# Kernel tuning notes

Measured on AMD Instinct MI355X. Metric: run time of the kernel, lower is better.

Reference implementation:

```python
import jax, jax.numpy as jnp
import numpy as np

B_, C, N, M, DX = 4, 8, 1024, 1024, 1
POINTS_PER_UNIT = 64


def setup_inputs() -> dict:
    key = jax.random.key(0)
    k1, k2, k3 = jax.random.split(key, 3)
    xz = jax.random.uniform(k1, (M, DX), dtype=jnp.float32)          # grid locations
    z = jax.random.normal(k2, (B_, C, M, M), dtype=jnp.float32)      # grid encoding
    x = jax.random.normal(k3, (B_, N, DX), dtype=jnp.float32)        # target locations
    log_scale = jnp.log(jnp.float32(2.0 / POINTS_PER_UNIT))          # learned scalar
    return {"xz": xz, "z": z, "x": x, "log_scale": log_scale}


def reference(xz, z, x, log_scale):
    # pairwise squared distances: (b, n, m)
    dists2 = jnp.sum((x[:, :, None, :] - xz[None, None, :, :]) ** 2, axis=-1)
    # RBF weights
    weights = jnp.exp(-0.5 * dists2 / jnp.exp(2.0 * log_scale))      # (b, n, m)
    # weighted interpolation of grid encoding: (b, c, n, m)
    z1 = jnp.einsum("bnm,bcmk->bcnk", weights, z)
    # outer product z1 @ z1^T: (b, c, n, n)
    z2 = jnp.einsum("bcnk,bcok->bcno", z1, z1)
    return (xz, z2)
```

## Files before the change

kernel.cpp:

```cpp
#include <hip/hip_runtime.h>
#include <hip/hip_bf16.h>


typedef __attribute__((ext_vector_type(8))) unsigned short u16x8;
typedef __attribute__((ext_vector_type(8))) __bf16 bf16x8;
typedef __attribute__((ext_vector_type(4))) float f32x4;

typedef __attribute__((address_space(1))) void gvoid;
typedef __attribute__((address_space(3))) void svoid;
#define GLDS(g, s) __builtin_amdgcn_global_load_lds((gvoid*)(g), (svoid*)(s), 16, 0, 0)
#define BAR() asm volatile("s_barrier" ::: "memory")

__device__ __forceinline__ unsigned short f2bf(float f) {
  unsigned int u = __builtin_bit_cast(unsigned int, f);
  u += 0x7fffu + ((u >> 16) & 1u);
  return (unsigned short)(u >> 16);
}

__device__ __forceinline__ bf16x8 as_bf16x8(u16x8 v) {
  return __builtin_bit_cast(bf16x8, v);
}

__global__ void weights_kernel(const float* __restrict__ xz, const float* __restrict__ x,
                               const float* __restrict__ ls, unsigned short* __restrict__ W) {
  int bn = blockIdx.x;
  float xv = x[bn];
  float coef = -0.5f * __expf(-2.0f * ls[0]);
  unsigned short* Wrow = W + (size_t)bn * 1024;
  #pragma unroll
  for (int i = 0; i < 4; ++i) {
    int m = threadIdx.x + i * 256;
    float d = xv - xz[m];
    Wrow[m] = f2bf(__expf(coef * d * d));
  }
}

__global__ void transpose_kernel(const float* __restrict__ Z, unsigned short* __restrict__ Zt) {
  __shared__ float tile[64][65];
  int bc = blockIdx.z;
  const float* Zp = Z + ((size_t)bc << 20);
  unsigned short* Ztp = Zt + ((size_t)bc << 20);
  int m0 = blockIdx.x * 64, k0 = blockIdx.y * 64;
  int tx = threadIdx.x & 63, tg = threadIdx.x >> 6;
  #pragma unroll
  for (int i = 0; i < 16; ++i) {
    int ml = tg + i * 4;
    tile[ml][tx] = Zp[(size_t)(m0 + ml) * 1024 + k0 + tx];
  }
  __syncthreads();
  int tx2 = (threadIdx.x & 31) * 2, kg = threadIdx.x >> 5;
  #pragma unroll
  for (int i = 0; i < 8; ++i) {
    int kl = kg + i * 8;
    ushort2 v;
    v.x = f2bf(tile[tx2][kl]);
    v.y = f2bf(tile[tx2 + 1][kl]);
    *(ushort2*)&Ztp[(size_t)(k0 + kl) * 1024 + m0 + tx2] = v;
  }
}

template<bool A_PER_B>
__global__ __launch_bounds__(512, 2)
void gemm_nt8(const unsigned short* __restrict__ A, const unsigned short* __restrict__ B,
              unsigned short* __restrict__ Cbf) {
  extern __shared__ __align__(16) char smem[];

  const int bid = blockIdx.x;
  const int w = ((bid & 7) << 6) + (bid >> 3);
  const int bc = w >> 4;
  const int t  = w & 15;
  const int bi = t & 3, bj = t >> 2;

  const unsigned short* Ap = A + ((size_t)(A_PER_B ? (bc >> 3) : bc) << 20);
  const unsigned short* Bp = B + ((size_t)bc << 20);
  const int tid = threadIdx.x;
  const int wv = tid >> 6, lane = tid & 63;
  const int wr = wv >> 2, wc = wv & 3;
  const int la = lane & 15, ha = lane >> 4;

  f32x4 acc[8][4] = {};

  const int slog = (lane & 7) ^ (lane >> 3);
  const int rloc = 2 * (lane >> 3) + (slog & 1);
  const int cloc = (slog >> 1) * 8;
  const unsigned short* gA0 = Ap + (size_t)(bi*256 +       wv*16 + rloc) * 1024 + cloc;
  const unsigned short* gA1 = Ap + (size_t)(bi*256 + 128 + wv*16 + rloc) * 1024 + cloc;
  const unsigned short* gB0 = Bp + (size_t)(bj*256 +       wv*16 + rloc) * 1024 + cloc;
  const unsigned short* gB1 = Bp + (size_t)(bj*256 + 128 + wv*16 + rloc) * 1024 + cloc;
  const int ldsw = wv * 1024;

  auto stageA = [&](int d, int kh, int kt) {
    const int ko = kt * 64 + kh * 32;
    char* dst = smem + d * 32768 + kh * 16384 + ldsw;
    GLDS(gA0 + ko, dst); GLDS(gA1 + ko, dst + 8192);
  };
  auto stageB = [&](int d, int kh, int kt) {
    const int ko = kt * 64 + kh * 32;
    char* dst = smem + 65536 + d * 32768 + kh * 16384 + ldsw;
    GLDS(gB0 + ko, dst); GLDS(gB1 + ko, dst + 8192);
  };

  const int sphys = ((ha << 1) | (la & 1)) ^ (la >> 1);
  const int abase = wr * 8192 + (la >> 1) * 128 + sphys * 16;
  const int bbase = 65536 + wc * 4096 + (la >> 1) * 128 + sphys * 16;

  u16x8 aX[4], aY[4], b0[4], b1[4];
  auto lda4 = [&](u16x8* dst, int d, int kh, int ms) {
    const char* p = smem + d * 32768 + kh * 16384 + ms * 4096 + abase;
    dst[0] = *(const u16x8*)(p);
    dst[1] = *(const u16x8*)(p + 1024);
    dst[2] = *(const u16x8*)(p + 2048);
    dst[3] = *(const u16x8*)(p + 3072);
  };
  auto ldb4 = [&](u16x8* dst, int d, int kh) {
    const char* p = smem + d * 32768 + kh * 16384 + bbase;
    dst[0] = *(const u16x8*)(p);
    dst[1] = *(const u16x8*)(p + 1024);
    dst[2] = *(const u16x8*)(p + 2048);
    dst[3] = *(const u16x8*)(p + 3072);
  };
  auto mfma16 = [&](const u16x8* Af, const u16x8* Bf, int ms) {
    #pragma unroll
    for (int i = 0; i < 4; ++i)
      #pragma unroll
      for (int n = 0; n < 4; ++n)
        acc[ms * 4 + i][n] = __builtin_amdgcn_mfma_f32_16x16x32_bf16(
            as_bf16x8(Af[i]), as_bf16x8(Bf[n]), acc[ms * 4 + i][n], 0, 0, 0);
  };

  stageA(0, 0, 0); stageB(0, 0, 0);
  stageA(0, 1, 0); stageB(0, 1, 0);
  stageA(1, 0, 1); stageB(1, 0, 1);
  asm volatile("s_waitcnt vmcnt(8)" ::: "memory");
  BAR();
  ldb4(b0, 0, 0); lda4(aX, 0, 0, 0);

  for (int tt = 0; tt < 14; ++tt) {
    const int d = tt & 1;
    stageA(d ^ 1, 1, tt + 1);
    lda4(aY, d, 0, 1);
    mfma16(aX, b0, 0);
    stageB(d ^ 1, 1, tt + 1);
    asm volatile("s_waitcnt vmcnt(8)" ::: "memory");
    BAR();
    ldb4(b1, d, 1); lda4(aX, d, 1, 0);
    mfma16(aY, b0, 1);
    stageA(d, 0, tt + 2);
    lda4(aY, d, 1, 1);
    mfma16(aX, b1, 0);
    stageB(d, 0, tt + 2);
    asm volatile("s_waitcnt vmcnt(8)" ::: "memory");
    BAR();
    ldb4(b0, d ^ 1, 0); lda4(aX, d ^ 1, 0, 0);
    mfma16(aY, b1, 1);
  }
  stageA(1, 1, 15);
  lda4(aY, 0, 0, 1);
  mfma16(aX, b0, 0);
  stageB(1, 1, 15);
  asm volatile("s_waitcnt vmcnt(8)" ::: "memory");
  BAR();
  ldb4(b1, 0, 1); lda4(aX, 0, 1, 0);
  mfma16(aY, b0, 1);
  lda4(aY, 0, 1, 1);
  mfma16(aX, b1, 0);
  asm volatile("s_waitcnt vmcnt(4)" ::: "memory");
  BAR();
  ldb4(b0, 1, 0); lda4(aX, 1, 0, 0);
  mfma16(aY, b1, 1);
  lda4(aY, 1, 0, 1);
  mfma16(aX, b0, 0);
  asm volatile("s_waitcnt vmcnt(0)" ::: "memory");
  BAR();
  ldb4(b1, 1, 1); lda4(aX, 1, 1, 0);
  mfma16(aY, b0, 1);
  lda4(aY, 1, 1, 1);
  mfma16(aX, b1, 0);
  mfma16(aY, b1, 1);
  BAR();

  const size_t cb20 = (size_t)bc << 20;
  unsigned short* sE = (unsigned short*)(smem) + wv * 1152;
  const int r2 = lane >> 2, ch = lane & 3;
  #pragma unroll
  for (int mb = 0; mb < 8; ++mb) {
    #pragma unroll
    for (int nb = 0; nb < 4; ++nb)
      #pragma unroll
      for (int j = 0; j < 4; ++j)
        sE[(ha * 4 + j) * 72 + nb * 16 + la] = f2bf(acc[mb][nb][j]);
    u16x8 v0 = *(const u16x8*)&sE[r2 * 72 + ch * 16];
    u16x8 v1 = *(const u16x8*)&sE[r2 * 72 + ch * 16 + 8];
    unsigned short* gp = Cbf + cb20 +
        (size_t)(bi * 256 + wr * 128 + mb * 16 + r2) * 1024 + bj * 256 + wc * 64 + ch * 16;
    *(u16x8*)gp = v0;
    *(u16x8*)(gp + 8) = v1;
  }
}

__global__ __launch_bounds__(256, 2)
void gemm2_sym(const unsigned short* __restrict__ A, float* __restrict__ Cf) {
  extern __shared__ __align__(16) char smem[];

  const int chunk = 144;
  int w = ((int)blockIdx.x & 7) * chunk + ((int)blockIdx.x >> 3);
  int bc = w / 36;
  int t  = w % 36;
  int bi = 0;
  while (t >= 8 - bi) { t -= 8 - bi; ++bi; }
  int bj = bi + t;

  const unsigned short* Ap = A + ((size_t)bc << 20);
  const int tid = threadIdx.x;
  const int wave = tid >> 6, lane = tid & 63;
  const int wr = wave >> 1, wc = wave & 1;
  const int la = lane & 15, ha = lane >> 4;
  f32x4 acc[4][4] = {};

  const int slog = (lane & 7) ^ (lane >> 3);
  const int rloc = 2 * (lane >> 3) + (slog & 1);
  const int cloc = (slog >> 1) * 8;
  const unsigned short* gA0 = Ap + (size_t)(bi*128 + (wave*2  )*16 + rloc)*1024 + cloc;
  const unsigned short* gA1 = Ap + (size_t)(bi*128 + (wave*2+1)*16 + rloc)*1024 + cloc;
  const unsigned short* gB0 = Ap + (size_t)(bj*128 + (wave*2  )*16 + rloc)*1024 + cloc;
  const unsigned short* gB1 = Ap + (size_t)(bj*128 + (wave*2+1)*16 + rloc)*1024 + cloc;
  const int ldsw = wave * 2048;

  auto stageA = [&](int d, int kh, int kt) {
    const int ko = kt * 64 + kh * 32;
    char* dst = smem + d * 32768 + kh * 8192 + ldsw;
    GLDS(gA0 + ko, dst); GLDS(gA1 + ko, dst + 1024);
  };
  auto stageB = [&](int d, int kh, int kt) {
    const int ko = kt * 64 + kh * 32;
    char* dst = smem + d * 32768 + 16384 + kh * 8192 + ldsw;
    GLDS(gB0 + ko, dst); GLDS(gB1 + ko, dst + 1024);
  };

  const int sphys = ((ha << 1) | (la & 1)) ^ (la >> 1);
  const int inv = (la >> 1) * 128 + sphys * 16;

  u16x8 aX[4], bX[4], aY[4], bY[4];
  auto lda4 = [&](u16x8* dst, int d, int kh) {
    const char* p = smem + d * 32768 + kh * 8192 + wr * 4096 + inv;
    dst[0] = *(const u16x8*)(p);
    dst[1] = *(const u16x8*)(p + 1024);
    dst[2] = *(const u16x8*)(p + 2048);
    dst[3] = *(const u16x8*)(p + 3072);
  };
  auto ldb4 = [&](u16x8* dst, int d, int kh) {
    const char* p = smem + d * 32768 + 16384 + kh * 8192 + wc * 4096 + inv;
    dst[0] = *(const u16x8*)(p);
    dst[1] = *(const u16x8*)(p + 1024);
    dst[2] = *(const u16x8*)(p + 2048);
    dst[3] = *(const u16x8*)(p + 3072);
  };
  auto mfma16 = [&](const u16x8* Af, const u16x8* Bf) {
    __builtin_amdgcn_s_setprio(1);
    #pragma unroll
    for (int m = 0; m < 4; ++m)
      #pragma unroll
      for (int n = 0; n < 4; ++n)
        acc[m][n] = __builtin_amdgcn_mfma_f32_16x16x32_bf16(
            as_bf16x8(Af[m]), as_bf16x8(Bf[n]), acc[m][n], 0, 0, 0);
    __builtin_amdgcn_s_setprio(0);
  };

  stageA(0, 0, 0); stageB(0, 0, 0);
  stageA(0, 1, 0); stageB(0, 1, 0);
  stageA(1, 0, 1); stageB(1, 0, 1);
  asm volatile("s_waitcnt vmcnt(8)" ::: "memory");
  BAR();
  lda4(aX, 0, 0); ldb4(bX, 0, 0);

  for (int tt = 0; tt < 14; ++tt) {
    const int d = tt & 1, e = d ^ 1;
    stageA(e, 1, tt + 1); stageB(e, 1, tt + 1);
    mfma16(aX, bX);
    asm volatile("s_waitcnt vmcnt(8)" ::: "memory");
    BAR();
    lda4(aY, d, 1); ldb4(bY, d, 1);
    stageA(d, 0, tt + 2); stageB(d, 0, tt + 2);
    mfma16(aY, bY);
    asm volatile("s_waitcnt vmcnt(8)" ::: "memory");
    BAR();
    lda4(aX, e, 0); ldb4(bX, e, 0);
  }
  stageA(1, 1, 15); stageB(1, 1, 15);
  mfma16(aX, bX);
  asm volatile("s_waitcnt vmcnt(8)" ::: "memory");
  BAR();
  lda4(aY, 0, 1); ldb4(bY, 0, 1);
  mfma16(aY, bY);
  asm volatile("s_waitcnt vmcnt(4)" ::: "memory");
  BAR();
  lda4(aX, 1, 0); ldb4(bX, 1, 0);
  mfma16(aX, bX);
  asm volatile("s_waitcnt vmcnt(0)" ::: "memory");
  BAR();
  lda4(aY, 1, 1); ldb4(bY, 1, 1);
  mfma16(aY, bY);
  BAR();

  const size_t cb20 = (size_t)bc << 20;

  #pragma unroll
  for (int m = 0; m < 4; ++m) {
    int row0 = bi * 128 + wr * 64 + m * 16 + ha * 4;
    #pragma unroll
    for (int n = 0; n < 4; ++n) {
      int col = bj * 128 + wc * 64 + n * 16 + la;
      #pragma unroll
      for (int j = 0; j < 4; ++j)
        Cf[cb20 + (size_t)(row0 + j) * 1024 + col] = acc[m][n][j];
    }
  }
  if (bi != bj) {
    float (*sT)[129] = (float(*)[129])smem;
    #pragma unroll
    for (int b = 0; b < 4; ++b) {
      if (wr == (b >> 1)) {
        #pragma unroll
        for (int dm = 0; dm < 2; ++dm) {
          int m = (b & 1) * 2 + dm;
          #pragma unroll
          for (int n = 0; n < 4; ++n)
            #pragma unroll
            for (int j = 0; j < 4; ++j)
              sT[dm * 16 + ha * 4 + j][wc * 64 + n * 16 + la] = acc[m][n][j];
        }
      }
      __syncthreads();
      int c  = tid >> 1;
      int r0 = (tid & 1) * 16;
      float* gp = Cf + cb20 + (size_t)(bj * 128 + c) * 1024 + bi * 128 + b * 32 + r0;
      #pragma unroll
      for (int q = 0; q < 4; ++q) {
        f32x4 v;
        #pragma unroll
        for (int k = 0; k < 4; ++k) v[k] = sT[r0 + q * 4 + k][c];
        *(f32x4*)(gp + q * 4) = v;
      }
      __syncthreads();
    }
  }
}

extern "C" void kernel_launch(void* const* d_in, const int* in_sizes, int n_in,
                              void* d_out, int out_size, void* d_ws, size_t ws_size,
                              hipStream_t stream) {
  const float* xz = (const float*)d_in[0];
  const float* z  = (const float*)d_in[1];
  const float* x  = (const float*)d_in[2];
  const float* ls = (const float*)d_in[3];
  float* out = (float*)d_out;

  unsigned short* W  = (unsigned short*)d_ws;
  unsigned short* Zt = W + ((size_t)4 << 20);
  unsigned short* z1 = Zt + ((size_t)32 << 20);

  hipFuncSetAttribute((const void*)gemm_nt8<true>,
                      hipFuncAttributeMaxDynamicSharedMemorySize, 131072);
  hipFuncSetAttribute((const void*)gemm2_sym,
                      hipFuncAttributeMaxDynamicSharedMemorySize, 65536);

  hipMemcpyAsync(out, xz, 1024 * sizeof(float), hipMemcpyDeviceToDevice, stream);
  weights_kernel<<<4096, 256, 0, stream>>>(xz, x, ls, W);
  transpose_kernel<<<dim3(16, 16, 32), 256, 0, stream>>>(z, Zt);
  gemm_nt8<true><<<512, 512, 131072, stream>>>(W, Zt, z1);
  gemm2_sym<<<32 * 36, 256, 65536, stream>>>(z1, out + 1024);
}
```

Baseline: 172.3 us.

## Load gemm2 A operand directly to registers and triple-buffer B in LDS

In the symmetric second GEMM, the A tile is no longer staged through shared memory. Each wave now loads its A fragments straight from global memory into registers, while only the B tile goes through LDS, in a rotating three-slot buffer. This shrinks dynamic LDS from 64KB to 48KB and raises the launch bound to 3 blocks per CU, aiming for more occupancy and less LDS traffic. The trade-off is that A fragment loads are strided global reads with more latency exposed on the MFMA critical path. It also relies on the reworked vmcnt accounting and on the epilogue's transpose scratch still fitting in the smaller LDS allocation.

```diff
diff --git a/kernel.cpp b/kernel.cpp
--- a/kernel.cpp
+++ b/kernel.cpp
@@ -198,7 +198,7 @@
   }
 }
 
-__global__ __launch_bounds__(256, 2)
+__global__ __launch_bounds__(256, 3)
 void gemm2_sym(const unsigned short* __restrict__ A, float* __restrict__ Cf) {
   extern __shared__ __align__(16) char smem[];
 
@@ -220,41 +220,35 @@
   const int slog = (lane & 7) ^ (lane >> 3);
   const int rloc = 2 * (lane >> 3) + (slog & 1);
   const int cloc = (slog >> 1) * 8;
-  const unsigned short* gA0 = Ap + (size_t)(bi*128 + (wave*2  )*16 + rloc)*1024 + cloc;
-  const unsigned short* gA1 = Ap + (size_t)(bi*128 + (wave*2+1)*16 + rloc)*1024 + cloc;
   const unsigned short* gB0 = Ap + (size_t)(bj*128 + (wave*2  )*16 + rloc)*1024 + cloc;
   const unsigned short* gB1 = Ap + (size_t)(bj*128 + (wave*2+1)*16 + rloc)*1024 + cloc;
   const int ldsw = wave * 2048;
 
-  auto stageA = [&](int d, int kh, int kt) {
-    const int ko = kt * 64 + kh * 32;
-    char* dst = smem + d * 32768 + kh * 8192 + ldsw;
-    GLDS(gA0 + ko, dst); GLDS(gA1 + ko, dst + 1024);
-  };
-  auto stageB = [&](int d, int kh, int kt) {
-    const int ko = kt * 64 + kh * 32;
-    char* dst = smem + d * 32768 + 16384 + kh * 8192 + ldsw;
-    GLDS(gB0 + ko, dst); GLDS(gB1 + ko, dst + 1024);
+  auto stageB = [&](int slot, int kt) {
+    const int ko = kt * 64;
+    char* dst = smem + slot * 16384 + ldsw;
+    GLDS(gB0 + ko,      dst);         GLDS(gB1 + ko,      dst + 1024);
+    GLDS(gB0 + ko + 32, dst + 8192);  GLDS(gB1 + ko + 32, dst + 9216);
+  };
+
+  const unsigned short* aG = Ap + (size_t)(bi * 128 + wr * 64 + la) * 1024 + ha * 8;
+  auto ldaG = [&](u16x8* dst, int kt, int kh) {
+    const unsigned short* p = aG + kt * 64 + kh * 32;
+    dst[0] = *(const u16x8*)(p);
+    dst[1] = *(const u16x8*)(p + 16384);
+    dst[2] = *(const u16x8*)(p + 32768);
+    dst[3] = *(const u16x8*)(p + 49152);
   };
 
   const int sphys = ((ha << 1) | (la & 1)) ^ (la >> 1);
   const int inv = (la >> 1) * 128 + sphys * 16;
-
-  u16x8 aX[4], bX[4], aY[4], bY[4];
-  auto lda4 = [&](u16x8* dst, int d, int kh) {
-    const char* p = smem + d * 32768 + kh * 8192 + wr * 4096 + inv;
+  auto ldbs = [&](u16x8* dst, int slot, int kh) {
+    const char* p = smem + slot * 16384 + kh * 8192 + wc * 4096 + inv;
     dst[0] = *(const u16x8*)(p);
     dst[1] = *(const u16x8*)(p + 1024);
     dst[2] = *(const u16x8*)(p + 2048);
     dst[3] = *(const u16x8*)(p + 3072);
   };
-  auto ldb4 = [&](u16x8* dst, int d, int kh) {
-    const char* p = smem + d * 32768 + 16384 + kh * 8192 + wc * 4096 + inv;
-    dst[0] = *(const u16x8*)(p);
-    dst[1] = *(const u16x8*)(p + 1024);
-    dst[2] = *(const u16x8*)(p + 2048);
-    dst[3] = *(const u16x8*)(p + 3072);
-  };
   auto mfma16 = [&](const u16x8* Af, const u16x8* Bf) {
     __builtin_amdgcn_s_setprio(1);
     #pragma unroll
@@ -266,40 +260,47 @@
     __builtin_amdgcn_s_setprio(0);
   };
 
-  stageA(0, 0, 0); stageB(0, 0, 0);
-  stageA(0, 1, 0); stageB(0, 1, 0);
-  stageA(1, 0, 1); stageB(1, 0, 1);
+  u16x8 aX[4], aY[4], bX[4], bY[4];
+
+  stageB(0, 0);
+  stageB(1, 1);
+  ldaG(aX, 0, 0);
   asm volatile("s_waitcnt vmcnt(8)" ::: "memory");
   BAR();
-  lda4(aX, 0, 0); ldb4(bX, 0, 0);
-
+  ldbs(bX, 0, 0);
+
+  int c0 = 0, c1 = 1, c2 = 2;
   for (int tt = 0; tt < 14; ++tt) {
-    const int d = tt & 1, e = d ^ 1;
-    stageA(e, 1, tt + 1); stageB(e, 1, tt + 1);
+    stageB(c2, tt + 2);
+    ldaG(aY, tt, 1);
     mfma16(aX, bX);
     asm volatile("s_waitcnt vmcnt(8)" ::: "memory");
     BAR();
-    lda4(aY, d, 1); ldb4(bY, d, 1);
-    stageA(d, 0, tt + 2); stageB(d, 0, tt + 2);
+    ldbs(bY, c0, 1);
+    ldaG(aX, tt + 1, 0);
     mfma16(aY, bY);
     asm volatile("s_waitcnt vmcnt(8)" ::: "memory");
     BAR();
-    lda4(aX, e, 0); ldb4(bX, e, 0);
-  }
-  stageA(1, 1, 15); stageB(1, 1, 15);
+    ldbs(bX, c1, 0);
+    int tmp = c0; c0 = c1; c1 = c2; c2 = tmp;
+  }
+  ldaG(aY, 14, 1);
   mfma16(aX, bX);
-  asm volatile("s_waitcnt vmcnt(8)" ::: "memory");
-  BAR();
-  lda4(aY, 0, 1); ldb4(bY, 0, 1);
+  asm volatile("s_waitcnt vmcnt(4)" ::: "memory");
+  BAR();
+  ldbs(bY, c0, 1);
+  ldaG(aX, 15, 0);
   mfma16(aY, bY);
   asm volatile("s_waitcnt vmcnt(4)" ::: "memory");
   BAR();
-  lda4(aX, 1, 0); ldb4(bX, 1, 0);
+  ldbs(bX, c1, 0);
+  ldaG(aY, 15, 1);
   mfma16(aX, bX);
+  asm volatile("s_waitcnt vmcnt(4)" ::: "memory");
+  BAR();
+  ldbs(bY, c1, 1);
+  mfma16(aY, bY);
   asm volatile("s_waitcnt vmcnt(0)" ::: "memory");
-  BAR();
-  lda4(aY, 1, 1); ldb4(bY, 1, 1);
-  mfma16(aY, bY);
   BAR();
 
   const size_t cb20 = (size_t)bc << 20;
@@ -362,11 +363,11 @@
   hipFuncSetAttribute((const void*)gemm_nt8<true>,
                       hipFuncAttributeMaxDynamicSharedMemorySize, 131072);
   hipFuncSetAttribute((const void*)gemm2_sym,
-                      hipFuncAttributeMaxDynamicSharedMemorySize, 65536);
+                      hipFuncAttributeMaxDynamicSharedMemorySize, 49152);
 
   hipMemcpyAsync(out, xz, 1024 * sizeof(float), hipMemcpyDeviceToDevice, stream);
   weights_kernel<<<4096, 256, 0, stream>>>(xz, x, ls, W);
   transpose_kernel<<<dim3(16, 16, 32), 256, 0, stream>>>(z, Zt);
   gemm_nt8<true><<<512, 512, 131072, stream>>>(W, Zt, z1);
-  gemm2_sym<<<32 * 36, 256, 65536, stream>>>(z1, out + 1024);
-}
+  gemm2_sym<<<32 * 36, 256, 49152, stream>>>(z1, out + 1024);
+}
```

Result: slower. 216.8 us (+25.8%).
